# Kernel optimization log

Measured on AMD Instinct MI355X. Metric: run time of the kernel, lower is better.

## Reference

```python
import jax, jax.numpy as jnp
import numpy as np

TOKENS, IN_F, OUT_F = 16384, 4096, 4096
Q_MAX_I8 = 127.0


def setup_inputs() -> dict:
    key = jax.random.key(0)
    k1, k2, k3, k4 = jax.random.split(key, 4)
    x = jax.random.normal(k1, (TOKENS, IN_F), dtype=jnp.float32)
    # packed int4 weights: two nibbles per byte along dim=1 -> [out, in//2]
    qweight = jax.random.randint(k2, (OUT_F, IN_F // 2), 0, 256, dtype=jnp.int32)
    # per-output-channel symmetric scale (positive)
    weight_scale = jax.random.uniform(k3, (OUT_F, 1), dtype=jnp.float32) * 0.01 + 1e-4
    bias = jax.random.normal(k4, (OUT_F,), dtype=jnp.float32)
    return {"x": x, "qweight": qweight, "weight_scale": weight_scale, "bias": bias}


def _unpack_int4(qweight):
    # high nibble -> even columns, low nibble -> odd columns (pack dim=1)
    high = (qweight >> 4) - 8            # [out, in//2], values in [-8, 7]
    low = (qweight & 15) - 8
    out_f = qweight.shape[0]
    return jnp.stack([high, low], axis=-1).reshape(out_f, -1)  # [out, in]


def reference(x, qweight, weight_scale, bias):
    # dequantize int4 weight: per-output-channel symmetric scale
    w = _unpack_int4(qweight).astype(jnp.float32) * weight_scale  # [out, in]
    # dynamic per-sample symmetric int8 activation fake-quant
    max_abs = jnp.max(jnp.abs(x), axis=-1, keepdims=True)         # [tokens, 1]
    act_scale = max_abs / Q_MAX_I8
    act_scale = jnp.where(act_scale == 0, 1.0, act_scale)
    q_x = jnp.clip(jnp.round(x / act_scale), -128.0, 127.0)
    x_dq = q_x * act_scale
    return x_dq @ w.T + bias
```

## Files before the change

kernel.cpp:

```cpp
#include <hip/hip_runtime.h>
#include <cstdint>

#define TOKENS 16384
#define IN_F   4096
#define OUT_F  4096

typedef int v4i __attribute__((ext_vector_type(4)));

__device__ __forceinline__ void async_lds16(const void* g, const void* l) {
    __builtin_amdgcn_global_load_lds(
        (const __attribute__((address_space(1))) void*)(uintptr_t)g,
        (__attribute__((address_space(3))) void*)(uint32_t)(uintptr_t)l,
        16, 0, 0);
}

__global__ __launch_bounds__(256) void act_quant_kernel(
        const float* __restrict__ x,
        signed char* __restrict__ qx,
        float* __restrict__ act_scale) {
    const int row = blockIdx.x;
    const int tid = threadIdx.x;
    const float4* xr = (const float4*)(x + (size_t)row * IN_F);

    float4 v[4];
    float m = 0.f;
#pragma unroll
    for (int i = 0; i < 4; ++i) {
        v[i] = xr[i * 256 + tid];
        m = fmaxf(m, fmaxf(fmaxf(fabsf(v[i].x), fabsf(v[i].y)),
                           fmaxf(fabsf(v[i].z), fabsf(v[i].w))));
    }
#pragma unroll
    for (int off = 32; off > 0; off >>= 1)
        m = fmaxf(m, __shfl_xor(m, off, 64));
    __shared__ float wmax[4];
    if ((tid & 63) == 0) wmax[tid >> 6] = m;
    __syncthreads();
    m = fmaxf(fmaxf(wmax[0], wmax[1]), fmaxf(wmax[2], wmax[3]));

    const float inv = (m == 0.f) ? 0.f : 127.0f / m;
    if (tid == 0) act_scale[row] = (m == 0.f) ? 1.0f : m / 127.0f;

    int* qr = (int*)(qx + (size_t)row * IN_F);
#pragma unroll
    for (int i = 0; i < 4; ++i) {
        int q0 = (int)fminf(fmaxf(rintf(v[i].x * inv), -128.f), 127.f);
        int q1 = (int)fminf(fmaxf(rintf(v[i].y * inv), -128.f), 127.f);
        int q2 = (int)fminf(fmaxf(rintf(v[i].z * inv), -128.f), 127.f);
        int q3 = (int)fminf(fmaxf(rintf(v[i].w * inv), -128.f), 127.f);
        qr[i * 256 + tid] = (q0 & 255) | ((q1 & 255) << 8) |
                            ((q2 & 255) << 16) | ((q3 & 255) << 24);
    }
}

__global__ __launch_bounds__(256) void unpack_w_kernel(
        const int* __restrict__ qw,
        signed char* __restrict__ w8) {
    const size_t idx = ((size_t)blockIdx.x * 256 + threadIdx.x) * 4;
    const int4 q = *(const int4*)(qw + idx);
    const int b0 = ((((q.x >> 4) & 15) - 8) & 255);
    const int b1 = (((q.x & 15) - 8) & 255);
    const int b2 = ((((q.y >> 4) & 15) - 8) & 255);
    const int b3 = (((q.y & 15) - 8) & 255);
    const int b4 = ((((q.z >> 4) & 15) - 8) & 255);
    const int b5 = (((q.z & 15) - 8) & 255);
    const int b6 = ((((q.w >> 4) & 15) - 8) & 255);
    const int b7 = (((q.w & 15) - 8) & 255);
    int2 d;
    d.x = b0 | (b1 << 8) | (b2 << 16) | (b3 << 24);
    d.y = b4 | (b5 << 8) | (b6 << 16) | (b7 << 24);
    *(int2*)(w8 + idx * 2) = d;
}

__global__ __launch_bounds__(256) void gemm_i8_kernel(
        const signed char* __restrict__ qx,
        const signed char* __restrict__ w8,
        const float* __restrict__ act_scale,
        const float* __restrict__ wscale,
        const float* __restrict__ bias,
        float* __restrict__ out) {
    __shared__ __align__(16) signed char sA[128 * 64];
    __shared__ __align__(16) signed char sB[128 * 64];

    const int nt = blockIdx.x & 31;
    const int mt = blockIdx.x >> 5;
    const int m0 = mt * 128, n0 = nt * 128;
    const int tid  = threadIdx.x;
    const int lane = tid & 63;
    const int wave = tid >> 6;
    const int wm = (wave >> 1) * 64;
    const int wn = (wave & 1) * 64;

    const int srow = wave * 32 + (lane >> 2);
    const int scol = (lane & 3) * 16;
    const signed char* gA = qx + (size_t)(m0 + srow) * IN_F + scol;
    const signed char* gB = w8 + (size_t)(n0 + srow) * IN_F + scol;
    signed char* lA = sA + wave * 2048;
    signed char* lB = sB + wave * 2048;

    v4i acc[4][4];
#pragma unroll
    for (int i = 0; i < 4; ++i)
#pragma unroll
        for (int j = 0; j < 4; ++j) acc[i][j] = (v4i){0, 0, 0, 0};

    const int frow = lane & 15;
    const int fcol = (lane >> 4) * 16;

    for (int k0 = 0; k0 < IN_F; k0 += 64) {
        __syncthreads();
        async_lds16(gA + k0,              lA);
        async_lds16(gA + k0 + 16 * IN_F,  lA + 1024);
        async_lds16(gB + k0,              lB);
        async_lds16(gB + k0 + 16 * IN_F,  lB + 1024);
        __syncthreads();

        v4i af[4], bf[4];
#pragma unroll
        for (int i = 0; i < 4; ++i)
            af[i] = *(const v4i*)(sA + (wm + i * 16 + frow) * 64 + fcol);
#pragma unroll
        for (int j = 0; j < 4; ++j)
            bf[j] = *(const v4i*)(sB + (wn + j * 16 + frow) * 64 + fcol);

#pragma unroll
        for (int i = 0; i < 4; ++i)
#pragma unroll
            for (int j = 0; j < 4; ++j)
                acc[i][j] = __builtin_amdgcn_mfma_i32_16x16x64_i8(
                    af[i], bf[j], acc[i][j], 0, 0, 0);
    }

    const int col_lane = lane & 15;
    const int row_q    = (lane >> 4) * 4;
    float4 as4[4];
#pragma unroll
    for (int i = 0; i < 4; ++i)
        as4[i] = *(const float4*)(act_scale + m0 + wm + i * 16 + row_q);

#pragma unroll
    for (int j = 0; j < 4; ++j) {
        const int n = n0 + wn + j * 16 + col_lane;
        const float wsn = wscale[n];
        const float bn  = bias[n];
#pragma unroll
        for (int i = 0; i < 4; ++i) {
            const int mb = m0 + wm + i * 16 + row_q;
            float* orow = out + (size_t)mb * OUT_F + n;
            const float* asp = (const float*)&as4[i];
#pragma unroll
            for (int r = 0; r < 4; ++r)
                orow[(size_t)r * OUT_F] = (float)acc[i][j][r] * (asp[r] * wsn) + bn;
        }
    }
}

extern "C" void kernel_launch(void* const* d_in, const int* in_sizes, int n_in,
                              void* d_out, int out_size, void* d_ws, size_t ws_size,
                              hipStream_t stream) {
    const float* x    = (const float*)d_in[0];
    const int*   qw   = (const int*)d_in[1];
    const float* wsc  = (const float*)d_in[2];
    const float* bias = (const float*)d_in[3];
    float* out = (float*)d_out;

    char* ws = (char*)d_ws;
    float*       act_scale = (float*)ws;
    signed char* qx        = (signed char*)(ws + 65536);
    signed char* w8        = (signed char*)(ws + 65536 + (size_t)TOKENS * IN_F);

    act_quant_kernel<<<TOKENS, 256, 0, stream>>>(x, qx, act_scale);
    unpack_w_kernel<<<(OUT_F * (IN_F / 2) / 4) / 256, 256, 0, stream>>>(qw, w8);
    gemm_i8_kernel<<<(TOKENS / 128) * (OUT_F / 128), 256, 0, stream>>>(
        qx, w8, act_scale, wsc, bias, out);
}
```

Before: 853.8 us.

## Widen int8 GEMM tile to 128x256 with fragment-ordered LDS layout

The GEMM block tile grows from 128x128 to 128x256, so each wave computes 64x128 with 32 accumulators, raising arithmetic intensity per LDS load and halving the grid. The LDS staging is also reorganized so each 16-row fragment is stored contiguously in MFMA-fragment order (lane*16), removing strided row addressing and likely LDS bank conflicts on fragment reads. The change doubles accumulator registers and LDS for B, which may lower occupancy, and it sets launch bounds with a minimum of 2 blocks.

```diff
diff --git a/kernel.cpp b/kernel.cpp
--- a/kernel.cpp
+++ b/kernel.cpp
@@ -72,7 +72,7 @@
     *(int2*)(w8 + idx * 2) = d;
 }
 
-__global__ __launch_bounds__(256) void gemm_i8_kernel(
+__global__ __launch_bounds__(256, 2) void gemm_i8_kernel(
         const signed char* __restrict__ qx,
         const signed char* __restrict__ w8,
         const float* __restrict__ act_scale,
@@ -80,53 +80,63 @@
         const float* __restrict__ bias,
         float* __restrict__ out) {
     __shared__ __align__(16) signed char sA[128 * 64];
-    __shared__ __align__(16) signed char sB[128 * 64];
+    __shared__ __align__(16) signed char sB[256 * 64];
 
-    const int nt = blockIdx.x & 31;
-    const int mt = blockIdx.x >> 5;
-    const int m0 = mt * 128, n0 = nt * 128;
+    const int nt = blockIdx.x & 15;
+    const int mt = blockIdx.x >> 4;
+    const int m0 = mt * 128, n0 = nt * 256;
     const int tid  = threadIdx.x;
     const int lane = tid & 63;
     const int wave = tid >> 6;
     const int wm = (wave >> 1) * 64;
-    const int wn = (wave & 1) * 64;
+    const int wn = (wave & 1) * 128;
 
-    const int srow = wave * 32 + (lane >> 2);
-    const int scol = (lane & 3) * 16;
-    const signed char* gA = qx + (size_t)(m0 + srow) * IN_F + scol;
-    const signed char* gB = w8 + (size_t)(n0 + srow) * IN_F + scol;
-    signed char* lA = sA + wave * 2048;
-    signed char* lB = sB + wave * 2048;
+    const int lrow = lane & 15;
+    const int lcol = (lane >> 4) * 16;
+    const signed char* gA0 = qx + (size_t)(m0 + 16 * (2 * wave)     + lrow) * IN_F + lcol;
+    const signed char* gA1 = qx + (size_t)(m0 + 16 * (2 * wave + 1) + lrow) * IN_F + lcol;
+    const signed char* gB0 = w8 + (size_t)(n0 + 16 * (4 * wave)     + lrow) * IN_F + lcol;
+    const signed char* gB1 = w8 + (size_t)(n0 + 16 * (4 * wave + 1) + lrow) * IN_F + lcol;
+    const signed char* gB2 = w8 + (size_t)(n0 + 16 * (4 * wave + 2) + lrow) * IN_F + lcol;
+    const signed char* gB3 = w8 + (size_t)(n0 + 16 * (4 * wave + 3) + lrow) * IN_F + lcol;
+    signed char* lA0 = sA + (2 * wave) * 1024;
+    signed char* lA1 = lA0 + 1024;
+    signed char* lB0 = sB + (4 * wave) * 1024;
+    signed char* lB1 = lB0 + 1024;
+    signed char* lB2 = lB0 + 2048;
+    signed char* lB3 = lB0 + 3072;
 
-    v4i acc[4][4];
+    v4i acc[4][8];
 #pragma unroll
     for (int i = 0; i < 4; ++i)
 #pragma unroll
-        for (int j = 0; j < 4; ++j) acc[i][j] = (v4i){0, 0, 0, 0};
+        for (int j = 0; j < 8; ++j) acc[i][j] = (v4i){0, 0, 0, 0};
 
-    const int frow = lane & 15;
-    const int fcol = (lane >> 4) * 16;
+    const signed char* fA = sA + (wm >> 4) * 1024 + lane * 16;
+    const signed char* fB = sB + (wn >> 4) * 1024 + lane * 16;
 
     for (int k0 = 0; k0 < IN_F; k0 += 64) {
         __syncthreads();
-        async_lds16(gA + k0,              lA);
-        async_lds16(gA + k0 + 16 * IN_F,  lA + 1024);
-        async_lds16(gB + k0,              lB);
-        async_lds16(gB + k0 + 16 * IN_F,  lB + 1024);
+        async_lds16(gA0 + k0, lA0);
+        async_lds16(gA1 + k0, lA1);
+        async_lds16(gB0 + k0, lB0);
+        async_lds16(gB1 + k0, lB1);
+        async_lds16(gB2 + k0, lB2);
+        async_lds16(gB3 + k0, lB3);
         __syncthreads();
 
-        v4i af[4], bf[4];
+        v4i af[4], bf[8];
 #pragma unroll
         for (int i = 0; i < 4; ++i)
-            af[i] = *(const v4i*)(sA + (wm + i * 16 + frow) * 64 + fcol);
+            af[i] = *(const v4i*)(fA + i * 1024);
 #pragma unroll
-        for (int j = 0; j < 4; ++j)
-            bf[j] = *(const v4i*)(sB + (wn + j * 16 + frow) * 64 + fcol);
+        for (int j = 0; j < 8; ++j)
+            bf[j] = *(const v4i*)(fB + j * 1024);
 
 #pragma unroll
         for (int i = 0; i < 4; ++i)
 #pragma unroll
-            for (int j = 0; j < 4; ++j)
+            for (int j = 0; j < 8; ++j)
                 acc[i][j] = __builtin_amdgcn_mfma_i32_16x16x64_i8(
                     af[i], bf[j], acc[i][j], 0, 0, 0);
     }
@@ -139,7 +149,7 @@
         as4[i] = *(const float4*)(act_scale + m0 + wm + i * 16 + row_q);
 
 #pragma unroll
-    for (int j = 0; j < 4; ++j) {
+    for (int j = 0; j < 8; ++j) {
         const int n = n0 + wn + j * 16 + col_lane;
         const float wsn = wscale[n];
         const float bn  = bias[n];
@@ -171,6 +181,6 @@
 
     act_quant_kernel<<<TOKENS, 256, 0, stream>>>(x, qx, act_scale);
     unpack_w_kernel<<<(OUT_F * (IN_F / 2) / 4) / 256, 256, 0, stream>>>(qw, w8);
-    gemm_i8_kernel<<<(TOKENS / 128) * (OUT_F / 128), 256, 0, stream>>>(
+    gemm_i8_kernel<<<(TOKENS / 128) * (OUT_F / 256), 256, 0, stream>>>(
         qx, w8, act_scale, wsc, bias, out);
 }
```

Result: no change. 849.4 us (-0.5%).
